# Performance work log

Measured on AMD Instinct MI355X. Metric: run time of the kernel, lower is better.

Reference implementation:

```python
import jax, jax.numpy as jnp
import numpy as np

B, S, D = 4, 4096, 256


def setup_inputs() -> dict:
    key = jax.random.key(0)
    ks = jax.random.split(key, 7)
    s = 1.0 / np.sqrt(D)
    return {
        "x": jax.random.normal(ks[0], (B, S, D), dtype=jnp.float32),
        "Wq": jax.random.uniform(ks[1], (D, D), jnp.float32, -s, s),
        "bq": jax.random.uniform(ks[2], (D,), jnp.float32, -s, s),
        "Wk": jax.random.uniform(ks[3], (D, D), jnp.float32, -s, s),
        "bk": jax.random.uniform(ks[4], (D,), jnp.float32, -s, s),
        "Wv": jax.random.uniform(ks[5], (D, D), jnp.float32, -s, s),
        "bv": jax.random.uniform(ks[6], (D,), jnp.float32, -s, s),
    }


def reference(x, Wq, bq, Wk, bk, Wv, bv):
    # nn.Linear: y = x @ W.T + b
    Q = jnp.einsum("bsd,ed->bse", x, Wq) + bq
    K = jnp.einsum("bsd,ed->bse", x, Wk) + bk
    V = jnp.einsum("bsd,ed->bse", x, Wv) + bv
    dk = Q.shape[-1]
    scores = jnp.einsum("bqd,bkd->bqk", Q, K) / jnp.sqrt(jnp.float32(dk))
    # NOTE: original applies softmax over dim=1 (the query axis), not -1.
    attn = jax.nn.softmax(scores, axis=1)
    out = jnp.einsum("bqk,bkd->bqd", attn, V)
    return out
```

## Files before the change

### kernel.cpp

```cpp
#include <hip/hip_runtime.h>

typedef short bf16x8 __attribute__((ext_vector_type(8)));
typedef float f32x4 __attribute__((ext_vector_type(4)));
typedef unsigned short u16;

#define S_LEN 4096
#define D_DIM 256
#define NROW  16384

__device__ __forceinline__ u16 f2bf(float f) {
    union { float f; unsigned u; } v; v.f = f;
    unsigned r = v.u + 0x7FFFu + ((v.u >> 16) & 1u);
    return (u16)(r >> 16);
}
__device__ __forceinline__ float bf2f(u16 h) {
    union { unsigned u; float f; } v; v.u = ((unsigned)h) << 16; return v.f;
}

__device__ __forceinline__ size_t fr_qk(int t, int kk) {
    return (size_t)t * 4096 + kk * 512;
}
__device__ __forceinline__ size_t fr_v(int p, int dt, int kk2) {
    return (size_t)p * 16384 + (dt * 2 + kk2) * 512;
}
__device__ __forceinline__ size_t e_base(int b, int kc, int qt) {
    return ((size_t)(b * 32768 + kc * 256 + qt)) * 512;
}

__device__ __forceinline__ void gll16(const u16* g, u16* l) {
    __builtin_amdgcn_global_load_lds(
        (const __attribute__((address_space(1))) unsigned int*)g,
        (__attribute__((address_space(3))) unsigned int*)l, 16, 0, 0);
}

#define WAITV4 asm volatile("s_waitcnt vmcnt(4)" ::: "memory")
#define WAITV0 asm volatile("s_waitcnt vmcnt(0)" ::: "memory")
#define WAITLGKM0 asm volatile("s_waitcnt lgkmcnt(0)" ::: "memory")
#define MEMFENCE asm volatile("" ::: "memory")

__global__ __launch_bounds__(256) void wconv(
    const float* __restrict__ Wq, const float* __restrict__ Wk,
    const float* __restrict__ Wv, u16* __restrict__ Wf)
{
    int i = blockIdx.x * 256 + threadIdx.x;
    int m = i >> 13;
    int idx = i & 8191;
    int ocol = idx >> 5;
    int d0 = (idx & 31) * 8;
    const float* s = (m == 0 ? Wq : (m == 1 ? Wk : Wv)) + ocol * 256 + d0;
    float4 v0 = *reinterpret_cast<const float4*>(s);
    float4 v1 = *reinterpret_cast<const float4*>(s + 4);
    union { ushort4 h[2]; int4 q; } t;
    t.h[0] = make_ushort4(f2bf(v0.x), f2bf(v0.y), f2bf(v0.z), f2bf(v0.w));
    t.h[1] = make_ushort4(f2bf(v1.x), f2bf(v1.y), f2bf(v1.z), f2bf(v1.w));
    size_t off = (size_t)m * 65536 + fr_qk(ocol >> 4, d0 >> 5)
               + ((d0 >> 3) & 3) * 128 + (ocol & 15) * 8;
    *reinterpret_cast<int4*>(Wf + off) = t.q;
}

__global__ __launch_bounds__(256) void qkv_proj(
    const float* __restrict__ x, const u16* __restrict__ Wf,
    const float* __restrict__ bq, const float* __restrict__ bk,
    const float* __restrict__ bv,
    u16* __restrict__ Qf, u16* __restrict__ Kf, u16* __restrict__ Vf)
{
    __shared__ u16 xs[32][264];
    const int tid = threadIdx.x;
    const int r0 = blockIdx.x * 32;

    #pragma unroll
    for (int i = 0; i < 8; ++i) {
        int c = i * 256 + tid;
        int row = c >> 6, c4 = c & 63;
        float4 v = reinterpret_cast<const float4*>(x + (size_t)(r0 + row) * D_DIM)[c4];
        *reinterpret_cast<ushort4*>(&xs[row][c4 * 4]) =
            make_ushort4(f2bf(v.x), f2bf(v.y), f2bf(v.z), f2bf(v.w));
    }
    __syncthreads();

    const int w = tid >> 6, l = tid & 63, lr = l & 15, lg = l >> 4;
    const int c0 = w * 64;

    bf16x8 a[2][8];
    #pragma unroll
    for (int qs = 0; qs < 2; ++qs)
        #pragma unroll
        for (int kk = 0; kk < 8; ++kk)
            a[qs][kk] = *reinterpret_cast<const bf16x8*>(&xs[qs * 16 + lr][kk * 32 + lg * 8]);

    const float* Bs[3] = {bq, bk, bv};

    #pragma unroll
    for (int m = 0; m < 3; ++m) {
        const u16* Wm = Wf + (size_t)m * 65536;
        f32x4 acc[2][4] = {};
        #pragma unroll
        for (int kk = 0; kk < 8; ++kk) {
            #pragma unroll
            for (int cf = 0; cf < 4; ++cf) {
                bf16x8 wfr = *reinterpret_cast<const bf16x8*>(
                    Wm + fr_qk(w * 4 + cf, kk) + l * 8);
                acc[0][cf] = __builtin_amdgcn_mfma_f32_16x16x32_bf16(a[0][kk], wfr, acc[0][cf], 0, 0, 0);
                acc[1][cf] = __builtin_amdgcn_mfma_f32_16x16x32_bf16(a[1][kk], wfr, acc[1][cf], 0, 0, 0);
            }
        }
        if (m < 2) {
            u16* outp = (m == 0) ? Qf : Kf;
            int t = r0 >> 4;
            #pragma unroll
            for (int qs = 0; qs < 2; ++qs) {
                #pragma unroll
                for (int cf = 0; cf < 4; ++cf) {
                    int col = c0 + cf * 16 + lr;
                    float bias = Bs[m][col];
                    size_t base = fr_qk(t + qs, col >> 5) + ((col >> 3) & 3) * 128 + (col & 7);
                    #pragma unroll
                    for (int r = 0; r < 4; ++r)
                        outp[base + (lg * 4 + r) * 8] = f2bf(acc[qs][cf][r] + bias);
                }
            }
        } else {
            int p  = (r0 >> 12) * 64 + ((r0 & 4095) >> 6);
            int kb = r0 & 63;
            #pragma unroll
            for (int qs = 0; qs < 2; ++qs) {
                #pragma unroll
                for (int cf = 0; cf < 4; ++cf) {
                    int d = c0 + cf * 16 + lr;
                    float bias = bv[d];
                    #pragma unroll
                    for (int r = 0; r < 4; ++r) {
                        int key = kb + qs * 16 + lg * 4 + r;
                        size_t off = fr_v(p, d >> 4, key >> 5)
                                   + ((key >> 3) & 3) * 128 + (d & 15) * 8 + (key & 7);
                        Vf[off] = f2bf(acc[qs][cf][r] + bias);
                    }
                }
            }
        }
    }
}

__global__ __launch_bounds__(256, 2) void score_exp(
    const u16* __restrict__ Qf, const u16* __restrict__ Kf,
    u16* __restrict__ Ef, float* __restrict__ Zp, int write_e)
{
    __shared__ __align__(16) u16 Qls[2][8192];
    const int tid = threadIdx.x, blk = blockIdx.x;
    const int xcd = blk & 7, sub = blk >> 3;
    const int b  = xcd >> 1;
    const int qq = ((xcd & 1) << 1) | (sub & 1);
    const int ktile = sub >> 1;
    const int w = tid >> 6, l = tid & 63, lr = l & 15, lg = l >> 4;
    const int k0 = ktile * 128;

    bf16x8 kreg[2][8];
    #pragma unroll
    for (int ks = 0; ks < 2; ++ks) {
        const int tk = b * 256 + (k0 >> 4) + w * 2 + ks;
        #pragma unroll
        for (int kk = 0; kk < 8; ++kk)
            kreg[ks][kk] = *reinterpret_cast<const bf16x8*>(Kf + fr_qk(tk, kk) + l * 8);
    }

    #define STAGE_Q(qt_, nb_) do { \
        const u16* g_ = Qf + ((size_t)(b * 256 + (qt_) * 2)) * 4096 + (w * 4) * 512 + l * 8; \
        u16* d_ = &Qls[nb_][(w * 4) * 512]; \
        _Pragma("unroll") \
        for (int f_ = 0; f_ < 4; ++f_) gll16(g_ + f_ * 512, d_ + f_ * 512); \
    } while (0)

    const int qt0 = qq * 32;
    STAGE_Q(qt0, 0);
    __syncthreads();

    float Z[2][4] = {};
    const float SC = 0.0625f;
    const int kc = ktile * 4 + w;

    for (int it = 0; it < 32; ++it) {
        const int cur = it & 1;
        if (it < 31) STAGE_Q(qt0 + it + 1, cur ^ 1);

        f32x4 acc[2][2] = {};
        #pragma unroll
        for (int kk = 0; kk < 8; ++kk) {
            #pragma unroll
            for (int qf = 0; qf < 2; ++qf) {
                bf16x8 qfr = *reinterpret_cast<const bf16x8*>(
                    &Qls[cur][(qf * 8 + kk) * 512 + l * 8]);
                acc[0][qf] = __builtin_amdgcn_mfma_f32_16x16x32_bf16(kreg[0][kk], qfr, acc[0][qf], 0, 0, 0);
                acc[1][qf] = __builtin_amdgcn_mfma_f32_16x16x32_bf16(kreg[1][kk], qfr, acc[1][qf], 0, 0, 0);
            }
        }
        #pragma unroll
        for (int ks = 0; ks < 2; ++ks) {
            #pragma unroll
            for (int qf = 0; qf < 2; ++qf) {
                float e0 = __expf(acc[ks][qf][0] * SC);
                float e1 = __expf(acc[ks][qf][1] * SC);
                float e2 = __expf(acc[ks][qf][2] * SC);
                float e3 = __expf(acc[ks][qf][3] * SC);
                Z[ks][0] += e0; Z[ks][1] += e1; Z[ks][2] += e2; Z[ks][3] += e3;
                if (write_e) {
                    size_t ad = e_base(b, kc, (qt0 + it) * 2 + qf)
                              + (ks * 2 + (lg >> 1)) * 128 + lr * 8 + (lg & 1) * 4;
                    *reinterpret_cast<ushort4*>(Ef + ad) =
                        make_ushort4(f2bf(e0), f2bf(e1), f2bf(e2), f2bf(e3));
                }
            }
        }
        __syncthreads();
    }

    #pragma unroll
    for (int ks = 0; ks < 2; ++ks) {
        #pragma unroll
        for (int r = 0; r < 4; ++r) {
            float z = Z[ks][r];
            z += __shfl_xor(z, 1);
            z += __shfl_xor(z, 2);
            z += __shfl_xor(z, 4);
            z += __shfl_xor(z, 8);
            if (lr == 0)
                Zp[qq * NROW + b * S_LEN + k0 + w * 32 + ks * 16 + lg * 4 + r] = z;
        }
    }
    #undef STAGE_Q
}

__global__ __launch_bounds__(256) void zrecip(
    const float* __restrict__ Zp, float* __restrict__ rZ)
{
    int i = blockIdx.x * 256 + threadIdx.x;
    rZ[i] = 1.0f / (((Zp[i] + Zp[NROW + i]) + Zp[2 * NROW + i]) + Zp[3 * NROW + i]);
}

__global__ __launch_bounds__(256) void zlog(
    const float* __restrict__ Zp, float* __restrict__ LZ)
{
    int i = blockIdx.x * 256 + threadIdx.x;
    LZ[i] = logf(((Zp[i] + Zp[NROW + i]) + Zp[2 * NROW + i]) + Zp[3 * NROW + i]);
}

__global__ __launch_bounds__(256) void vscale(
    u16* __restrict__ Vf, const float* __restrict__ rZ)
{
    int i = blockIdx.x * 256 + threadIdx.x;
    int frag = i >> 6, l8 = i & 63;
    int p = frag >> 5, sub = frag & 31, kk2 = sub & 1;
    int b = p >> 6, kt = p & 63;
    int kbase = b * S_LEN + kt * 64 + kk2 * 32 + (l8 >> 4) * 8;
    float4 rz0 = *reinterpret_cast<const float4*>(&rZ[kbase]);
    float4 rz1 = *reinterpret_cast<const float4*>(&rZ[kbase + 4]);
    ushort4* vp = reinterpret_cast<ushort4*>(Vf + (size_t)i * 8);
    ushort4 a = vp[0], c = vp[1];
    vp[0] = make_ushort4(f2bf(bf2f(a.x) * rz0.x), f2bf(bf2f(a.y) * rz0.y),
                         f2bf(bf2f(a.z) * rz0.z), f2bf(bf2f(a.w) * rz0.w));
    vp[1] = make_ushort4(f2bf(bf2f(c.x) * rz1.x), f2bf(bf2f(c.y) * rz1.y),
                         f2bf(bf2f(c.z) * rz1.z), f2bf(bf2f(c.w) * rz1.w));
}

__global__ __launch_bounds__(256, 4) void pv_gemm(
    const u16* __restrict__ Ef, const u16* __restrict__ Vf, float* __restrict__ out)
{
    __shared__ __align__(16) u16 Vls[2][8192];

    const int tid = threadIdx.x, blk = blockIdx.x;
    const int xcd = blk & 7, sub = blk >> 3;
    const int b  = xcd >> 1;
    const int ks = ((xcd & 1) << 1) | (sub & 1);
    const int qt64 = sub >> 1;
    const int w = tid >> 6, l = tid & 63, lr = l & 15, lg = l >> 4;
    const int qh = w & 1, dh = w >> 1;

    #define EADDR(it_, j_) \
        (Ef + e_base(b, ks * 32 + (it_), qt64 * 4 + qh * 2 + (j_)) + l * 8)

    #define STAGE_V(it_, nb_) do { \
        const int kc_ = ks * 32 + (it_); \
        const size_t vb_ = ((size_t)(b * 64 + (kc_ >> 1))) * 16384 + (kc_ & 1) * 512; \
        _Pragma("unroll") \
        for (int f_ = 0; f_ < 4; ++f_) { \
            int dt_ = w * 4 + f_; \
            gll16(Vf + vb_ + (size_t)(dt_ * 2) * 512 + l * 8, &Vls[nb_][dt_ * 512]); \
        } \
    } while (0)

    #define COMPUTE(nb_, e0_, e1_) do { \
        __builtin_amdgcn_s_setprio(1); \
        _Pragma("unroll") \
        for (int dt = 0; dt < 8; ++dt) { \
            bf16x8 vfr = *reinterpret_cast<const bf16x8*>( \
                &Vls[nb_][(dh * 8 + dt) * 512 + l * 8]); \
            acc[0][dt] = __builtin_amdgcn_mfma_f32_16x16x32_bf16(e0_, vfr, acc[0][dt], 0, 0, 0); \
            acc[1][dt] = __builtin_amdgcn_mfma_f32_16x16x32_bf16(e1_, vfr, acc[1][dt], 0, 0, 0); \
        } \
        __builtin_amdgcn_s_setprio(0); \
    } while (0)

    f32x4 acc[2][8] = {};
    bf16x8 eA0, eA1, eB0, eB1;

    eA0 = *reinterpret_cast<const bf16x8*>(EADDR(0, 0));
    eA1 = *reinterpret_cast<const bf16x8*>(EADDR(0, 1));
    STAGE_V(0, 0);
    WAITV0;
    __builtin_amdgcn_s_barrier();
    MEMFENCE;

    #pragma unroll 1
    for (int it = 0; it < 30; it += 2) {
        eB0 = *reinterpret_cast<const bf16x8*>(EADDR(it + 1, 0));
        eB1 = *reinterpret_cast<const bf16x8*>(EADDR(it + 1, 1));
        STAGE_V(it + 1, 1);
        COMPUTE(0, eA0, eA1);
        WAITV0;
        __builtin_amdgcn_s_barrier();
        MEMFENCE;
        eA0 = *reinterpret_cast<const bf16x8*>(EADDR(it + 2, 0));
        eA1 = *reinterpret_cast<const bf16x8*>(EADDR(it + 2, 1));
        STAGE_V(it + 2, 0);
        COMPUTE(1, eB0, eB1);
        WAITV0;
        __builtin_amdgcn_s_barrier();
        MEMFENCE;
    }
    eB0 = *reinterpret_cast<const bf16x8*>(EADDR(31, 0));
    eB1 = *reinterpret_cast<const bf16x8*>(EADDR(31, 1));
    STAGE_V(31, 1);
    COMPUTE(0, eA0, eA1);
    WAITV0;
    __builtin_amdgcn_s_barrier();
    MEMFENCE;
    COMPUTE(1, eB0, eB1);

    const int qg = b * S_LEN + qt64 * 64 + qh * 32;
    const int dg = dh * 128;
    #pragma unroll
    for (int qf = 0; qf < 2; ++qf) {
        #pragma unroll
        for (int dt = 0; dt < 8; ++dt) {
            #pragma unroll
            for (int r = 0; r < 4; ++r) {
                unsafeAtomicAdd(&out[(size_t)(qg + qf * 16 + lg * 4 + r) * D_DIM
                                     + dg + dt * 16 + lr],
                                acc[qf][dt][r]);
            }
        }
    }
    #undef EADDR
    #undef STAGE_V
    #undef COMPUTE
}

__global__ __launch_bounds__(512, 1) void attn_out_fb(
    const u16* __restrict__ Qf, const u16* __restrict__ Kf, const u16* __restrict__ Vf,
    const float* __restrict__ LZ, float* __restrict__ out)
{
    __shared__ __align__(16) u16 Kls[3][8192];
    __shared__ __align__(16) u16 Vls[4][8192];
    __shared__ __align__(16) u16 ps[8][2][1280];
    __shared__ __align__(16) float lzs[1024];

    const int tid = threadIdx.x, blk = blockIdx.x;
    const int xcd = blk & 7, sub = blk >> 3;
    const int b  = xcd >> 1;
    const int kq = ((xcd & 1) << 1) | (sub & 1);
    const int qtile = sub >> 1;
    const int w = tid >> 6, l = tid & 63, lr = l & 15, lg = l >> 4;
    const int q0 = qtile * 256 + w * 32;
    const int base_tk = b * 256;
    const int kt0 = kq * 32;

    bf16x8 qreg[2][8];
    #pragma unroll
    for (int qs = 0; qs < 2; ++qs) {
        const int tq = base_tk + ((q0 + qs * 16) >> 4);
        #pragma unroll
        for (int kk = 0; kk < 8; ++kk)
            qreg[qs][kk] = *reinterpret_cast<const bf16x8*>(Qf + fr_qk(tq, kk) + l * 8);
    }

    #define STAGE(kt_) do { \
        if (w < 4) { \
            const u16* g_ = Kf + ((size_t)(base_tk + (kt0 + (kt_)) * 2)) * 4096 + (w * 4) * 512 + l * 8; \
            u16* d_ = &Kls[(kt_) % 3][(w * 4) * 512]; \
            _Pragma("unroll") \
            for (int f_ = 0; f_ < 4; ++f_) gll16(g_ + f_ * 512, d_ + f_ * 512); \
        } else { \
            const int kta_ = kt0 + (kt_); \
            const size_t vb_ = ((size_t)(b * 64 + (kta_ >> 1))) * 16384 + (kta_ & 1) * 512; \
            const int dt0_ = (w - 4) * 4; \
            _Pragma("unroll") \
            for (int f_ = 0; f_ < 4; ++f_) \
                gll16(Vf + vb_ + (size_t)(dt0_ + f_) * 1024 + l * 8, &Vls[(kt_) % 4][(dt0_ + f_) * 512]); \
        } \
    } while (0)

    #define QK(kt_) do { \
        const u16* kb_ = &Kls[(kt_) % 3][0]; \
        __builtin_amdgcn_s_setprio(1); \
        _Pragma("unroll") \
        for (int kk = 0; kk < 8; ++kk) { \
            bf16x8 k0_ = *reinterpret_cast<const bf16x8*>(kb_ + kk * 512 + l * 8); \
            bf16x8 k1_ = *reinterpret_cast<const bf16x8*>(kb_ + (8 + kk) * 512 + l * 8); \
            sacc[0][0] = __builtin_amdgcn_mfma_f32_16x16x32_bf16(qreg[0][kk], k0_, sacc[0][0], 0, 0, 0); \
            sacc[0][1] = __builtin_amdgcn_mfma_f32_16x16x32_bf16(qreg[1][kk], k0_, sacc[0][1], 0, 0, 0); \
            sacc[1][0] = __builtin_amdgcn_mfma_f32_16x16x32_bf16(qreg[0][kk], k1_, sacc[1][0], 0, 0, 0); \
            sacc[1][1] = __builtin_amdgcn_mfma_f32_16x16x32_bf16(qreg[1][kk], k1_, sacc[1][1], 0, 0, 0); \
        } \
        __builtin_amdgcn_s_setprio(0); \
    } while (0)

    #define PV(j_) do { \
        const u16* vb_ = &Vls[(j_) % 4][0]; \
        const u16* pb_ = &ps[w][(j_) & 1][0]; \
        bf16x8 af0_ = *reinterpret_cast<const bf16x8*>(pb_ + lr * 40 + lg * 8); \
        bf16x8 af1_ = *reinterpret_cast<const bf16x8*>(pb_ + (16 + lr) * 40 + lg * 8); \
        __builtin_amdgcn_s_setprio(1); \
        _Pragma("unroll") \
        for (int dt = 0; dt < 16; ++dt) { \
            bf16x8 vf_ = *reinterpret_cast<const bf16x8*>(vb_ + dt * 512 + l * 8); \
            oacc[0][dt] = __builtin_amdgcn_mfma_f32_16x16x32_bf16(af0_, vf_, oacc[0][dt], 0, 0, 0); \
            oacc[1][dt] = __builtin_amdgcn_mfma_f32_16x16x32_bf16(af1_, vf_, oacc[1][dt], 0, 0, 0); \
        } \
        __builtin_amdgcn_s_setprio(0); \
    } while (0)

    #define SM(kt_) do { \
        u16* pw_ = &ps[w][(kt_) & 1][0]; \
        _Pragma("unroll") \
        for (int cf = 0; cf < 2; ++cf) { \
            float Lv_ = lzs[(kt_) * 32 + cf * 16 + lr]; \
            _Pragma("unroll") \
            for (int qs = 0; qs < 2; ++qs) \
                _Pragma("unroll") \
                for (int r = 0; r < 4; ++r) { \
                    float p_ = __expf(fmaf(sacc[cf][qs][r], SC, -Lv_)); \
                    pw_[(qs * 16 + lg * 4 + r) * 40 + cf * 16 + lr] = f2bf(p_); \
                } \
        } \
    } while (0)

    f32x4 oacc[2][16] = {};
    const float SC = 0.0625f;

    f32x4 lzv;
    if (tid < 256)
        lzv = *reinterpret_cast<const f32x4*>(LZ + b * S_LEN + kt0 * 32 + tid * 4);
    STAGE(0);
    STAGE(1);
    if (tid < 256)
        *reinterpret_cast<f32x4*>(&lzs[tid * 4]) = lzv;
    WAITLGKM0;
    WAITV4;
    __builtin_amdgcn_s_barrier();
    MEMFENCE;

    #pragma unroll 1
    for (int kt = 0; kt < 30; ++kt) {
        STAGE(kt + 2);
        f32x4 sacc[2][2] = {};
        QK(kt);
        if (kt > 0) PV(kt - 1);
        SM(kt);
        WAITV4;
        __builtin_amdgcn_s_barrier();
        MEMFENCE;
    }
    {
        f32x4 sacc[2][2] = {};
        QK(30); PV(29); SM(30);
        WAITV0;
        __builtin_amdgcn_s_barrier();
        MEMFENCE;
    }
    {
        f32x4 sacc[2][2] = {};
        QK(31); PV(30); SM(31); PV(31);
    }

    #pragma unroll
    for (int qs = 0; qs < 2; ++qs) {
        #pragma unroll
        for (int dt = 0; dt < 16; ++dt) {
            #pragma unroll
            for (int r = 0; r < 4; ++r) {
                int row = q0 + qs * 16 + lg * 4 + r;
                unsafeAtomicAdd(&out[((size_t)(b * S_LEN + row)) * D_DIM + dt * 16 + lr],
                                oacc[qs][dt][r]);
            }
        }
    }
    #undef STAGE
    #undef QK
    #undef PV
    #undef SM
}

extern "C" void kernel_launch(void* const* d_in, const int* in_sizes, int n_in,
                              void* d_out, int out_size, void* d_ws, size_t ws_size,
                              hipStream_t stream) {
    const float* x  = (const float*)d_in[0];
    const float* Wq = (const float*)d_in[1];
    const float* bq = (const float*)d_in[2];
    const float* Wk = (const float*)d_in[3];
    const float* bk = (const float*)d_in[4];
    const float* Wv = (const float*)d_in[5];
    const float* bv = (const float*)d_in[6];
    float* out = (float*)d_out;

    u16* Qf = (u16*)d_ws;
    u16* Kf = Qf + (size_t)NROW * D_DIM;
    u16* Vf = Kf + (size_t)NROW * D_DIM;
    u16* Wf = Vf + (size_t)NROW * D_DIM;
    float* Zp = (float*)(Wf + 196608);
    float* rZ = Zp + 4 * NROW;
    u16* Ef = (u16*)(rZ + NROW);

    const size_t need = (size_t)((char*)Ef - (char*)d_ws) + (size_t)4 * 32768 * 512 * 2;

    hipMemsetAsync(out, 0, (size_t)NROW * D_DIM * sizeof(float), stream);
    wconv<<<96, 256, 0, stream>>>(Wq, Wk, Wv, Wf);
    qkv_proj<<<NROW / 32, 256, 0, stream>>>(x, Wf, bq, bk, bv, Qf, Kf, Vf);

    if (ws_size >= need) {
        score_exp<<<512, 256, 0, stream>>>(Qf, Kf, Ef, Zp, 1);
        zrecip<<<NROW / 256, 256, 0, stream>>>(Zp, rZ);
        vscale<<<2048, 256, 0, stream>>>(Vf, rZ);
        pv_gemm<<<1024, 256, 0, stream>>>(Ef, Vf, out);
    } else {
        score_exp<<<512, 256, 0, stream>>>(Qf, Kf, Qf , Zp, 0);
        zlog<<<NROW / 256, 256, 0, stream>>>(Zp, rZ);
        attn_out_fb<<<256, 512, 0, stream>>>(Qf, Kf, Vf, rZ, out);
    }
}
```

Measured before the change: 166.3 us.

## Deepen E-fragment prefetch to two iterations with partial vmcnt wait

Restructures the main loop of the attention-output kernel so the E register fragments are prefetched two iterations ahead using a three-register rotation. The per-iteration wait becomes vmcnt(2) instead of vmcnt(0), so the in-flight E loads no longer stall the barrier. The intent is to hide global load latency behind MFMA compute. It costs extra registers, and the correctness of the vmcnt counting depends on the order in which loads are issued.

```diff
diff --git a/kernel.cpp b/kernel.cpp
--- a/kernel.cpp
+++ b/kernel.cpp
@@ -34,6 +34,7 @@
 }
 
 #define WAITV4 asm volatile("s_waitcnt vmcnt(4)" ::: "memory")
+#define WAITV2 asm volatile("s_waitcnt vmcnt(2)" ::: "memory")
 #define WAITV0 asm volatile("s_waitcnt vmcnt(0)" ::: "memory")
 #define WAITLGKM0 asm volatile("s_waitcnt lgkmcnt(0)" ::: "memory")
 #define MEMFENCE asm volatile("" ::: "memory")
@@ -299,35 +300,39 @@
         __builtin_amdgcn_s_setprio(0); \
     } while (0)
 
+    #define BODY(it_, eC0_, eC1_, eN0_, eN1_) do { \
+        STAGE_V((it_) + 1, ((it_) + 1) & 1); \
+        MEMFENCE; \
+        eN0_ = *reinterpret_cast<const bf16x8*>(EADDR((it_) + 2, 0)); \
+        eN1_ = *reinterpret_cast<const bf16x8*>(EADDR((it_) + 2, 1)); \
+        MEMFENCE; \
+        COMPUTE((it_) & 1, eC0_, eC1_); \
+        WAITV2; \
+        __builtin_amdgcn_s_barrier(); \
+        MEMFENCE; \
+    } while (0)
+
     f32x4 acc[2][8] = {};
-    bf16x8 eA0, eA1, eB0, eB1;
+    bf16x8 eA0, eA1, eB0, eB1, eC0, eC1;
 
     eA0 = *reinterpret_cast<const bf16x8*>(EADDR(0, 0));
     eA1 = *reinterpret_cast<const bf16x8*>(EADDR(0, 1));
+    MEMFENCE;
     STAGE_V(0, 0);
-    WAITV0;
+    MEMFENCE;
+    eB0 = *reinterpret_cast<const bf16x8*>(EADDR(1, 0));
+    eB1 = *reinterpret_cast<const bf16x8*>(EADDR(1, 1));
+    MEMFENCE;
+    WAITV2;
     __builtin_amdgcn_s_barrier();
     MEMFENCE;
 
     #pragma unroll 1
-    for (int it = 0; it < 30; it += 2) {
-        eB0 = *reinterpret_cast<const bf16x8*>(EADDR(it + 1, 0));
-        eB1 = *reinterpret_cast<const bf16x8*>(EADDR(it + 1, 1));
-        STAGE_V(it + 1, 1);
-        COMPUTE(0, eA0, eA1);
-        WAITV0;
-        __builtin_amdgcn_s_barrier();
-        MEMFENCE;
-        eA0 = *reinterpret_cast<const bf16x8*>(EADDR(it + 2, 0));
-        eA1 = *reinterpret_cast<const bf16x8*>(EADDR(it + 2, 1));
-        STAGE_V(it + 2, 0);
-        COMPUTE(1, eB0, eB1);
-        WAITV0;
-        __builtin_amdgcn_s_barrier();
-        MEMFENCE;
-    }
-    eB0 = *reinterpret_cast<const bf16x8*>(EADDR(31, 0));
-    eB1 = *reinterpret_cast<const bf16x8*>(EADDR(31, 1));
+    for (int base = 0; base < 30; base += 3) {
+        BODY(base,     eA0, eA1, eC0, eC1);
+        BODY(base + 1, eB0, eB1, eA0, eA1);
+        BODY(base + 2, eC0, eC1, eB0, eB1);
+    }
     STAGE_V(31, 1);
     COMPUTE(0, eA0, eA1);
     WAITV0;
@@ -352,6 +357,7 @@
     #undef EADDR
     #undef STAGE_V
     #undef COMPUTE
+    #undef BODY
 }
 
 __global__ __launch_bounds__(512, 1) void attn_out_fb(
```

Result: no change. 164.5 us (-1.1%).
